# Kernel tuning notes

Measured on AMD Instinct MI355X. Metric: run time of the kernel, lower is better.

Reference implementation:

```python
import jax, jax.numpy as jnp
import numpy as np

EMBED = 2048
HEADS = 16
HEAD_DIM = EMBED // HEADS


def setup_inputs() -> dict:
    key = jax.random.key(0)
    ks = jax.random.split(key, 9)
    s = 1.0 / np.sqrt(EMBED)
    inp = {"x": jax.random.normal(ks[0], (2, 2048, EMBED), dtype=jnp.float32)}
    for i, name in enumerate(["q", "k", "v", "o"]):
        inp[f"W{name}"] = jax.random.uniform(ks[1 + 2 * i], (EMBED, EMBED), dtype=jnp.float32, minval=-s, maxval=s)
        inp[f"b{name}"] = jax.random.uniform(ks[2 + 2 * i], (EMBED,), dtype=jnp.float32, minval=-s, maxval=s)
    return inp


def reference(x, Wq, bq, Wk, bk, Wv, bv, Wo, bo):
    B, S, E = x.shape
    def split_heads(t):
        return t.reshape(B, S, HEADS, HEAD_DIM).transpose(0, 2, 1, 3)  # [B,H,S,D]
    q = split_heads(x @ Wq.T + bq)
    k = split_heads(x @ Wk.T + bk)
    v = split_heads(x @ Wv.T + bv)
    scale = 1.0 / np.sqrt(HEAD_DIM)
    scores = jnp.einsum("bhqd,bhkd->bhqk", q, k) * scale  # [B,H,S,S]
    causal = jnp.tril(jnp.ones((S, S), dtype=bool))
    scores = jnp.where(causal[None, None], scores, -jnp.inf)
    attn = jax.nn.softmax(scores, axis=-1)
    out = jnp.einsum("bhqk,bhkd->bhqd", attn, v)  # [B,H,S,D]
    out = out.transpose(0, 2, 1, 3).reshape(B, S, E)
    return out @ Wo.T + bo
```

## Files before the change

### kernel.cpp

```cpp
#include <hip/hip_runtime.h>

typedef unsigned short u16;
typedef unsigned int u32;
typedef __attribute__((ext_vector_type(8))) short bf16x8;
typedef __attribute__((ext_vector_type(4))) float f32x4;

#define MFMA(a, b, c) __builtin_amdgcn_mfma_f32_16x16x32_bf16((a), (b), (c), 0, 0, 0)

__device__ inline u16 f2bf(float f) {
  u32 u = __float_as_uint(f);
  u = (u + 0x7fffu + ((u >> 16) & 1u)) >> 16;
  return (u16)u;
}

__device__ inline void gld16(u16* lds, const u16* g) {
  __builtin_amdgcn_global_load_lds((const __attribute__((address_space(1))) void*)g,
                                   (__attribute__((address_space(3))) void*)lds,
                                   16, 0, 0);
}

__global__ __launch_bounds__(256) void cvt_all(const float* __restrict__ x,
                                               const float* __restrict__ wa,
                                               const float* __restrict__ wb,
                                               const float* __restrict__ wc,
                                               const float* __restrict__ wd,
                                               uint2* __restrict__ dst) {
  int i = blockIdx.x * 256 + threadIdx.x;
  const float* s;
  int off;
  if (i < 2097152) {
    s = x; off = i;
  } else {
    int j = i - 2097152;
    int which = j >> 20;
    off = j & 1048575;
    s = (which == 0) ? wa : (which == 1) ? wb : (which == 2) ? wc : wd;
  }
  float4 f = ((const float4*)s)[off];
  u32 lo = (u32)f2bf(f.x) | ((u32)f2bf(f.y) << 16);
  u32 hi = (u32)f2bf(f.z) | ((u32)f2bf(f.w) << 16);
  dst[i] = make_uint2(lo, hi);
}

__device__ inline void gemm_core(const u16* __restrict__ A, const u16* __restrict__ W,
                                 u16* As, u16* Bs, int m0, int n0, f32x4 acc[4][4]) {
  const int K = 2048;
  const int NT = 64;
  int t = threadIdx.x, w = t >> 6, l = t & 63;
  int wr = (w >> 1) * 64, wc = (w & 1) * 64;
  int fr = l & 15, fg = l >> 4;
  int r0 = t >> 2;
  int r1 = 64 + r0;
  int c00 = (t & 3) ^ ((r0 >> 1) & 3);
  int c01 = (t & 3) ^ ((r1 >> 1) & 3);
  const u16* gA = A + (size_t)m0 * K;
  const u16* gB = W + (size_t)n0 * K;
  size_t a0 = (size_t)r0 * K + c00 * 8;
  size_t a1 = (size_t)r1 * K + c01 * 8;
#pragma unroll
  for (int p = 0; p < 2; ++p) {
    u16* sa = As + p * 4096;
    u16* sb = Bs + p * 4096;
    int kk = p * 32;
    gld16(sa + w * 512, gA + a0 + kk);
    gld16(sa + 2048 + w * 512, gA + a1 + kk);
    gld16(sb + w * 512, gB + a0 + kk);
    gld16(sb + 2048 + w * 512, gB + a1 + kk);
  }
  for (int kt = 0; kt < NT; ++kt) {
    int kt2 = (kt + 2 < NT) ? (kt + 2) : (NT - 1);
    u16* sa = As + ((kt + 2) & 3) * 4096;
    u16* sb = Bs + ((kt + 2) & 3) * 4096;
    int kk = kt2 * 32;
    gld16(sa + w * 512, gA + a0 + kk);
    gld16(sa + 2048 + w * 512, gA + a1 + kk);
    gld16(sb + w * 512, gB + a0 + kk);
    gld16(sb + 2048 + w * 512, gB + a1 + kk);
    asm volatile("s_waitcnt vmcnt(8)\n\ts_barrier" ::: "memory");
    const u16* ca = As + (kt & 3) * 4096;
    const u16* cb = Bs + (kt & 3) * 4096;
    bf16x8 af[4], bfv[4];
#pragma unroll
    for (int i = 0; i < 4; ++i) {
      int ar = wr + i * 16 + fr;
      af[i] = *(const bf16x8*)&ca[ar * 32 + ((fg ^ ((ar >> 1) & 3)) << 3)];
    }
#pragma unroll
    for (int i = 0; i < 4; ++i) {
      int br = wc + i * 16 + fr;
      bfv[i] = *(const bf16x8*)&cb[br * 32 + ((fg ^ ((br >> 1) & 3)) << 3)];
    }
    __builtin_amdgcn_s_setprio(1);
#pragma unroll
    for (int mi = 0; mi < 4; ++mi)
#pragma unroll
      for (int ni = 0; ni < 4; ++ni)
        acc[mi][ni] = MFMA(af[mi], bfv[ni], acc[mi][ni]);
    __builtin_amdgcn_s_setprio(0);
  }
}

__global__ __launch_bounds__(512, 2) void qkv_gemm(
    const u16* __restrict__ X, const u16* __restrict__ Wq, const u16* __restrict__ Wk,
    const u16* __restrict__ Wv, const float* __restrict__ bq, const float* __restrict__ bk,
    const float* __restrict__ bv, u16* __restrict__ Qo, u16* __restrict__ Ko,
    u16* __restrict__ Vo) {
  __shared__ __attribute__((aligned(16))) u16 As[32768];
  __shared__ __attribute__((aligned(16))) u16 Bs[32768];
  const int K = 2048, NT = 64;
  int which = blockIdx.x >> 3;
  int n0 = (blockIdx.x & 7) * 256;
  int m0 = blockIdx.y * 256;
  const u16* W = (which == 0) ? Wq : (which == 1) ? Wk : Wv;
  const float* bias = (which == 0) ? bq : (which == 1) ? bk : bv;
  u16* out = (which == 0) ? Qo : (which == 1) ? Ko : Vo;
  float scale = (which == 0) ? 0.08838834764831845f : 1.0f;
  int t = threadIdx.x, w = t >> 6, l = t & 63;
  int wm = w >> 2, wn = w & 3;
  int fr = l & 15, fg = l >> 4;
  int r0 = t >> 2;
  int c0 = (t & 3) ^ ((r0 >> 1) & 3);
  const u16* gA = X + (size_t)m0 * K;
  const u16* gB = W + (size_t)n0 * K;
  size_t a0 = (size_t)r0 * K + c0 * 8;
  size_t a1 = a0 + (size_t)128 * K;
  f32x4 zero4 = {0.f, 0.f, 0.f, 0.f};
  f32x4 acc[8][4];
#pragma unroll
  for (int i = 0; i < 8; ++i)
#pragma unroll
    for (int j = 0; j < 4; ++j) acc[i][j] = zero4;
#pragma unroll
  for (int p = 0; p < 2; ++p) {
    u16* sa = As + p * 8192;
    u16* sb = Bs + p * 8192;
    int kk = p * 32;
    gld16(sa + w * 512, gA + a0 + kk);
    gld16(sa + 4096 + w * 512, gA + a1 + kk);
    gld16(sb + w * 512, gB + a0 + kk);
    gld16(sb + 4096 + w * 512, gB + a1 + kk);
  }
  asm volatile("s_waitcnt vmcnt(4)" ::: "memory");
  __builtin_amdgcn_s_barrier();
  for (int kt = 0; kt < NT; ++kt) {
    int kt2 = (kt + 2 < NT) ? (kt + 2) : (NT - 1);
    u16* sa = As + ((kt + 2) & 3) * 8192;
    u16* sb = Bs + ((kt + 2) & 3) * 8192;
    int kk = kt2 * 32;
    const u16* ca = As + (kt & 3) * 8192;
    const u16* cb = Bs + (kt & 3) * 8192;
    bf16x8 af[8], bfv[4];
#pragma unroll
    for (int i = 0; i < 4; ++i) {
      int ar = wm * 128 + i * 16 + fr;
      af[i] = *(const bf16x8*)&ca[ar * 32 + ((fg ^ ((ar >> 1) & 3)) << 3)];
    }
#pragma unroll
    for (int i = 0; i < 4; ++i) {
      int br = wn * 64 + i * 16 + fr;
      bfv[i] = *(const bf16x8*)&cb[br * 32 + ((fg ^ ((br >> 1) & 3)) << 3)];
    }
    gld16(sa + w * 512, gA + a0 + kk);
    gld16(sa + 4096 + w * 512, gA + a1 + kk);
    __builtin_amdgcn_s_barrier();
    __builtin_amdgcn_sched_barrier(0);
    __builtin_amdgcn_s_setprio(1);
#pragma unroll
    for (int mi = 0; mi < 4; ++mi)
#pragma unroll
      for (int ni = 0; ni < 4; ++ni)
        acc[mi][ni] = MFMA(af[mi], bfv[ni], acc[mi][ni]);
    __builtin_amdgcn_s_setprio(0);
    __builtin_amdgcn_sched_barrier(0);
    __builtin_amdgcn_s_barrier();
#pragma unroll
    for (int i = 4; i < 8; ++i) {
      int ar = wm * 128 + i * 16 + fr;
      af[i] = *(const bf16x8*)&ca[ar * 32 + ((fg ^ ((ar >> 1) & 3)) << 3)];
    }
    gld16(sb + w * 512, gB + a0 + kk);
    gld16(sb + 4096 + w * 512, gB + a1 + kk);
    __builtin_amdgcn_s_barrier();
    __builtin_amdgcn_sched_barrier(0);
    __builtin_amdgcn_s_setprio(1);
#pragma unroll
    for (int mi = 4; mi < 8; ++mi)
#pragma unroll
      for (int ni = 0; ni < 4; ++ni)
        acc[mi][ni] = MFMA(af[mi], bfv[ni], acc[mi][ni]);
    __builtin_amdgcn_s_setprio(0);
    __builtin_amdgcn_sched_barrier(0);
    asm volatile("s_waitcnt vmcnt(4)" ::: "memory");
    __builtin_amdgcn_s_barrier();
  }
  if (which == 2) {
#pragma unroll
    for (int mi = 0; mi < 8; ++mi) {
#pragma unroll
      for (int ni = 0; ni < 4; ++ni) {
        int row = m0 + wm * 128 + mi * 16 + (l >> 4) * 4;
        int col = n0 + wn * 64 + ni * 16 + (l & 15);
        float bb = bias[col];
        int h = col >> 7, d = col & 127;
        int b = row >> 11, s = row & 2047;
        u32 p0 = (u32)f2bf(acc[mi][ni][0] + bb) | ((u32)f2bf(acc[mi][ni][1] + bb) << 16);
        u32 p1 = (u32)f2bf(acc[mi][ni][2] + bb) | ((u32)f2bf(acc[mi][ni][3] + bb) << 16);
        *(uint2*)&out[((size_t)(b * 16 + h) * 128 + d) * 2048 + s] = make_uint2(p0, p1);
      }
    }
  } else {
#pragma unroll
    for (int mi = 0; mi < 8; ++mi) {
#pragma unroll
      for (int ni = 0; ni < 4; ++ni) {
        int row = m0 + wm * 128 + mi * 16 + (l >> 4) * 4;
        int col = n0 + wn * 64 + ni * 16 + (l & 15);
        float bb = bias[col];
        int h = col >> 7, d = col & 127;
#pragma unroll
        for (int i = 0; i < 4; ++i) {
          int m = row + i;
          int b = m >> 11, s = m & 2047;
          float v = (acc[mi][ni][i] + bb) * scale;
          out[(((size_t)b * 16 + h) * 2048 + s) * 128 + d] = f2bf(v);
        }
      }
    }
  }
}

__global__ __launch_bounds__(256, 2) void oproj_gemm(const u16* __restrict__ A,
                                                     const u16* __restrict__ W,
                                                     const float* __restrict__ bias,
                                                     float* __restrict__ out) {
  __shared__ __attribute__((aligned(16))) u16 As[16384];
  __shared__ __attribute__((aligned(16))) u16 Bs[16384];
  int n0 = blockIdx.x * 128, m0 = blockIdx.y * 128;
  f32x4 zero4 = {0.f, 0.f, 0.f, 0.f};
  f32x4 acc[4][4];
#pragma unroll
  for (int i = 0; i < 4; ++i)
#pragma unroll
    for (int j = 0; j < 4; ++j) acc[i][j] = zero4;
  gemm_core(A, W, As, Bs, m0, n0, acc);
  int t = threadIdx.x, w = t >> 6, l = t & 63;
  int wr = (w >> 1) * 64, wc = (w & 1) * 64;
#pragma unroll
  for (int mi = 0; mi < 4; ++mi) {
#pragma unroll
    for (int ni = 0; ni < 4; ++ni) {
      int row = m0 + wr + mi * 16 + (l >> 4) * 4;
      int col = n0 + wc + ni * 16 + (l & 15);
      float bb = bias[col];
#pragma unroll
      for (int i = 0; i < 4; ++i) out[(size_t)(row + i) * 2048 + col] = acc[mi][ni][i] + bb;
    }
  }
}

__global__ __launch_bounds__(256, 2) void attn_fwd(const u16* __restrict__ Q,
                                                   const u16* __restrict__ K,
                                                   const u16* __restrict__ Vt,
                                                   u16* __restrict__ AO) {
  __shared__ __attribute__((aligned(16))) u16 Ks[8192];
  __shared__ __attribute__((aligned(16))) u16 Vts[8192];
  __shared__ __attribute__((aligned(16))) u16 Pl[8192];
  const int D = 128;
  int b3 = blockIdx.x;
  int bh = b3 & 31;
  int xq = b3 >> 5;
  int qt = (xq < 8) ? (15 - xq) : (xq - 8);
  int t = threadIdx.x, w = t >> 6, l = t & 63, g = l >> 4, c = l & 15;
  size_t base = (size_t)bh * 2048 * 128;
  const u16* Vbh = Vt + base;
  int q0 = qt * 128;
  int qrw = q0 + w * 32;
  bf16x8 qf[2][4];
#pragma unroll
  for (int mi = 0; mi < 2; ++mi) {
    const u16* qp = Q + base + (size_t)(qrw + mi * 16 + c) * D + g * 8;
#pragma unroll
    for (int ks = 0; ks < 4; ++ks) qf[mi][ks] = *(const bf16x8*)(qp + ks * 32);
  }
  f32x4 zero4 = {0.f, 0.f, 0.f, 0.f};
  f32x4 oacc[2][8];
#pragma unroll
  for (int mi = 0; mi < 2; ++mi)
#pragma unroll
    for (int i = 0; i < 8; ++i) oacc[mi][i] = zero4;
  float mrow[2][4], lrow[2][4];
#pragma unroll
  for (int mi = 0; mi < 2; ++mi)
#pragma unroll
    for (int i = 0; i < 4; ++i) { mrow[mi][i] = -1e30f; lrow[mi][i] = 0.f; }
  char* pw = (char*)(Pl + w * 2048);
  int ktmax = 2 * qt + 1;
  for (int kt = 0; kt <= ktmax; ++kt) {
    int kv0 = kt * 64;
    __syncthreads();
#pragma unroll
    for (int ci = 0; ci < 4; ++ci) {
      int row = w * 16 + ci * 4 + g;
      int cc = c ^ (row & 7);
      gld16(Ks + w * 2048 + ci * 512, K + base + (size_t)(kv0 + row) * D + cc * 8);
    }
#pragma unroll
    for (int ci = 0; ci < 4; ++ci) {
      int vr = ci * 32 + w * 8 + (l >> 3);
      int vslot = (l & 7) ^ ((l >> 3) & 7);
      gld16(Vts + ci * 2048 + w * 512, Vbh + (size_t)vr * 2048 + kv0 + vslot * 8);
    }
    __syncthreads();
    if (kv0 <= qrw + 31) {
      f32x4 sacc[2][4];
#pragma unroll
      for (int mi = 0; mi < 2; ++mi)
#pragma unroll
        for (int n = 0; n < 4; ++n) sacc[mi][n] = zero4;
#pragma unroll
      for (int ks = 0; ks < 4; ++ks) {
#pragma unroll
        for (int n = 0; n < 4; ++n) {
          int row = n * 16 + c;
          bf16x8 kf = *(const bf16x8*)&Ks[row * 128 + (((ks * 4 + g) ^ (c & 7)) << 3)];
          sacc[0][n] = MFMA(qf[0][ks], kf, sacc[0][n]);
          sacc[1][n] = MFMA(qf[1][ks], kf, sacc[1][n]);
        }
      }
      float sc[2][4][4];
#pragma unroll
      for (int mi = 0; mi < 2; ++mi)
#pragma unroll
        for (int n = 0; n < 4; ++n)
#pragma unroll
          for (int i = 0; i < 4; ++i) sc[mi][n][i] = sacc[mi][n][i];
      if (kv0 + 63 > qrw) {
#pragma unroll
        for (int mi = 0; mi < 2; ++mi)
#pragma unroll
          for (int n = 0; n < 4; ++n) {
            int kv = kv0 + n * 16 + c;
#pragma unroll
            for (int i = 0; i < 4; ++i)
              if (kv > qrw + mi * 16 + g * 4 + i) sc[mi][n][i] = -1e30f;
          }
      }
      float tmax[2][4];
#pragma unroll
      for (int mi = 0; mi < 2; ++mi)
#pragma unroll
        for (int i = 0; i < 4; ++i)
          tmax[mi][i] = fmaxf(fmaxf(sc[mi][0][i], sc[mi][1][i]), fmaxf(sc[mi][2][i], sc[mi][3][i]));
#pragma unroll
      for (int x = 1; x < 16; x <<= 1)
#pragma unroll
        for (int mi = 0; mi < 2; ++mi)
#pragma unroll
          for (int i = 0; i < 4; ++i) tmax[mi][i] = fmaxf(tmax[mi][i], __shfl_xor(tmax[mi][i], x));
      float corr[2][4], rs[2][4];
#pragma unroll
      for (int mi = 0; mi < 2; ++mi)
#pragma unroll
        for (int i = 0; i < 4; ++i) {
          float mn = fmaxf(mrow[mi][i], tmax[mi][i]);
          corr[mi][i] = __expf(mrow[mi][i] - mn);
          mrow[mi][i] = mn;
          rs[mi][i] = 0.f;
        }
      float ps[2][4][4];
#pragma unroll
      for (int mi = 0; mi < 2; ++mi)
#pragma unroll
        for (int n = 0; n < 4; ++n)
#pragma unroll
          for (int i = 0; i < 4; ++i) {
            ps[mi][n][i] = __expf(sc[mi][n][i] - mrow[mi][i]);
            rs[mi][i] += ps[mi][n][i];
          }
#pragma unroll
      for (int x = 1; x < 16; x <<= 1)
#pragma unroll
        for (int mi = 0; mi < 2; ++mi)
#pragma unroll
          for (int i = 0; i < 4; ++i) rs[mi][i] += __shfl_xor(rs[mi][i], x);
#pragma unroll
      for (int mi = 0; mi < 2; ++mi)
#pragma unroll
        for (int i = 0; i < 4; ++i) lrow[mi][i] = lrow[mi][i] * corr[mi][i] + rs[mi][i];
#pragma unroll
      for (int mi = 0; mi < 2; ++mi)
#pragma unroll
        for (int nf = 0; nf < 8; ++nf)
#pragma unroll
          for (int i = 0; i < 4; ++i) oacc[mi][nf][i] *= corr[mi][i];
#pragma unroll
      for (int mi = 0; mi < 2; ++mi)
#pragma unroll
        for (int n = 0; n < 4; ++n)
#pragma unroll
          for (int i = 0; i < 4; ++i) {
            int row = mi * 16 + g * 4 + i;
            *(u16*)(pw + row * 128 + ((n * 32 + c * 2) ^ ((row & 7) << 4))) = f2bf(ps[mi][n][i]);
          }
#pragma unroll
      for (int ks = 0; ks < 2; ++ks) {
        bf16x8 pf0 = *(const bf16x8*)(pw + (c)*128 + ((ks * 64 + g * 16) ^ ((c & 7) << 4)));
        bf16x8 pf1 = *(const bf16x8*)(pw + (16 + c) * 128 + ((ks * 64 + g * 16) ^ ((c & 7) << 4)));
#pragma unroll
        for (int nf = 0; nf < 8; ++nf) {
          bf16x8 vf = *(const bf16x8*)&Vts[(nf * 16 + c) * 64 + (((ks * 4 + g) ^ (c & 7)) << 3)];
          oacc[0][nf] = MFMA(pf0, vf, oacc[0][nf]);
          oacc[1][nf] = MFMA(pf1, vf, oacc[1][nf]);
        }
      }
    }
  }
  int b = bh >> 4, h = bh & 15;
#pragma unroll
  for (int mi = 0; mi < 2; ++mi)
#pragma unroll
    for (int nf = 0; nf < 8; ++nf) {
      int d = h * 128 + nf * 16 + c;
#pragma unroll
      for (int i = 0; i < 4; ++i) {
        int q = qrw + mi * 16 + g * 4 + i;
        AO[((size_t)b * 2048 + q) * 2048 + d] = f2bf(oacc[mi][nf][i] / lrow[mi][i]);
      }
    }
}

extern "C" void kernel_launch(void* const* d_in, const int* in_sizes, int n_in,
                              void* d_out, int out_size, void* d_ws, size_t ws_size,
                              hipStream_t stream) {
  const float* x = (const float*)d_in[0];
  const float* Wq = (const float*)d_in[1];
  const float* bq = (const float*)d_in[2];
  const float* Wk = (const float*)d_in[3];
  const float* bk = (const float*)d_in[4];
  const float* Wv = (const float*)d_in[5];
  const float* bv = (const float*)d_in[6];
  const float* Wo = (const float*)d_in[7];
  const float* bo = (const float*)d_in[8];
  float* out = (float*)d_out;

  u16* xb = (u16*)d_ws;
  u16* Wqb = xb + 8388608;
  u16* Wkb = Wqb + 4194304;
  u16* Wvb = Wkb + 4194304;
  u16* Wob = Wvb + 4194304;
  u16* Qb = Wob + 4194304;
  u16* Kb = Qb + 8388608;
  u16* Vb = Kb + 8388608;
  u16* AOb = xb;

  cvt_all<<<24576, 256, 0, stream>>>(x, Wq, Wk, Wv, Wo, (uint2*)d_ws);
  qkv_gemm<<<dim3(24, 16), 512, 0, stream>>>(xb, Wqb, Wkb, Wvb, bq, bk, bv, Qb, Kb, Vb);
  attn_fwd<<<512, 256, 0, stream>>>(Qb, Kb, Vb, AOb);
  oproj_gemm<<<dim3(16, 32), 256, 0, stream>>>(AOb, Wob, bo, out);
}
```

Before: 288.2 us.

## Restructure QKV GEMM main loop into double-buffered 64-wide K steps

The QKV projection GEMM main loop now covers 64 K-elements per iteration as two 32-wide sub-steps, and uses two LDS halves in ping-pong order instead of a four-slot ring with prefetch distance two. The A-fragment register array shrinks from 8 to 4 entries and is reloaded for the upper rows, which lowers register pressure. Explicit lgkmcnt waits are placed before each MFMA block, and the vmcnt wait moves to sit after each B prefetch. The goal is fewer loop iterations and less bookkeeping. In exchange the prefetch distance is shorter and there are more barriers per iteration.

```diff
diff --git a/kernel.cpp b/kernel.cpp
--- a/kernel.cpp
+++ b/kernel.cpp
@@ -107,7 +107,7 @@
     u16* __restrict__ Vo) {
   __shared__ __attribute__((aligned(16))) u16 As[32768];
   __shared__ __attribute__((aligned(16))) u16 Bs[32768];
-  const int K = 2048, NT = 64;
+  const int K = 2048, NT = 32;
   int which = blockIdx.x >> 3;
   int n0 = (blockIdx.x & 7) * 256;
   int m0 = blockIdx.y * 256;
@@ -118,8 +118,8 @@
   int t = threadIdx.x, w = t >> 6, l = t & 63;
   int wm = w >> 2, wn = w & 3;
   int fr = l & 15, fg = l >> 4;
-  int r0 = t >> 2;
-  int c0 = (t & 3) ^ ((r0 >> 1) & 3);
+  int r0 = t >> 2, sl = t & 3;
+  int c0 = sl ^ ((r0 >> 1) & 3);
   const u16* gA = X + (size_t)m0 * K;
   const u16* gB = W + (size_t)n0 * K;
   size_t a0 = (size_t)r0 * K + c0 * 8;
@@ -130,26 +130,23 @@
   for (int i = 0; i < 8; ++i)
 #pragma unroll
     for (int j = 0; j < 4; ++j) acc[i][j] = zero4;
-#pragma unroll
-  for (int p = 0; p < 2; ++p) {
-    u16* sa = As + p * 8192;
-    u16* sb = Bs + p * 8192;
-    int kk = p * 32;
-    gld16(sa + w * 512, gA + a0 + kk);
-    gld16(sa + 4096 + w * 512, gA + a1 + kk);
-    gld16(sb + w * 512, gB + a0 + kk);
-    gld16(sb + 4096 + w * 512, gB + a1 + kk);
-  }
+  gld16(As + w * 512, gA + a0);
+  gld16(As + 4096 + w * 512, gA + a1);
+  gld16(Bs + w * 512, gB + a0);
+  gld16(Bs + 4096 + w * 512, gB + a1);
+  gld16(As + 8192 + w * 512, gA + a0 + 32);
+  gld16(As + 8192 + 4096 + w * 512, gA + a1 + 32);
+  gld16(Bs + 8192 + w * 512, gB + a0 + 32);
+  gld16(Bs + 8192 + 4096 + w * 512, gB + a1 + 32);
   asm volatile("s_waitcnt vmcnt(4)" ::: "memory");
   __builtin_amdgcn_s_barrier();
-  for (int kt = 0; kt < NT; ++kt) {
-    int kt2 = (kt + 2 < NT) ? (kt + 2) : (NT - 1);
-    u16* sa = As + ((kt + 2) & 3) * 8192;
-    u16* sb = Bs + ((kt + 2) & 3) * 8192;
-    int kk = kt2 * 32;
-    const u16* ca = As + (kt & 3) * 8192;
-    const u16* cb = Bs + (kt & 3) * 8192;
-    bf16x8 af[8], bfv[4];
+  for (int T = 0; T < NT; ++T) {
+    const u16* ca = As + (T & 1) * 16384;
+    const u16* cb = Bs + (T & 1) * 16384;
+    int Ts = (T + 1 < NT) ? (T + 1) : T;
+    int so = ((T + 1) & 1) * 16384;
+    size_t gk = (size_t)Ts * 64;
+    bf16x8 af[4], bfv[4];
 #pragma unroll
     for (int i = 0; i < 4; ++i) {
       int ar = wm * 128 + i * 16 + fr;
@@ -160,9 +157,10 @@
       int br = wn * 64 + i * 16 + fr;
       bfv[i] = *(const bf16x8*)&cb[br * 32 + ((fg ^ ((br >> 1) & 3)) << 3)];
     }
-    gld16(sa + w * 512, gA + a0 + kk);
-    gld16(sa + 4096 + w * 512, gA + a1 + kk);
-    __builtin_amdgcn_s_barrier();
+    gld16(As + so + w * 512, gA + a0 + gk);
+    gld16(As + so + 4096 + w * 512, gA + a1 + gk);
+    __builtin_amdgcn_s_barrier();
+    asm volatile("s_waitcnt lgkmcnt(0)" ::: "memory");
     __builtin_amdgcn_sched_barrier(0);
     __builtin_amdgcn_s_setprio(1);
 #pragma unroll
@@ -174,23 +172,68 @@
     __builtin_amdgcn_sched_barrier(0);
     __builtin_amdgcn_s_barrier();
 #pragma unroll
-    for (int i = 4; i < 8; ++i) {
+    for (int i = 0; i < 4; ++i) {
+      int ar = wm * 128 + (i + 4) * 16 + fr;
+      af[i] = *(const bf16x8*)&ca[ar * 32 + ((fg ^ ((ar >> 1) & 3)) << 3)];
+    }
+    gld16(Bs + so + w * 512, gB + a0 + gk);
+    gld16(Bs + so + 4096 + w * 512, gB + a1 + gk);
+    asm volatile("s_waitcnt vmcnt(4)" ::: "memory");
+    __builtin_amdgcn_s_barrier();
+    asm volatile("s_waitcnt lgkmcnt(0)" ::: "memory");
+    __builtin_amdgcn_sched_barrier(0);
+    __builtin_amdgcn_s_setprio(1);
+#pragma unroll
+    for (int mi = 0; mi < 4; ++mi)
+#pragma unroll
+      for (int ni = 0; ni < 4; ++ni)
+        acc[mi + 4][ni] = MFMA(af[mi], bfv[ni], acc[mi + 4][ni]);
+    __builtin_amdgcn_s_setprio(0);
+    __builtin_amdgcn_sched_barrier(0);
+    __builtin_amdgcn_s_barrier();
+#pragma unroll
+    for (int i = 0; i < 4; ++i) {
       int ar = wm * 128 + i * 16 + fr;
-      af[i] = *(const bf16x8*)&ca[ar * 32 + ((fg ^ ((ar >> 1) & 3)) << 3)];
-    }
-    gld16(sb + w * 512, gB + a0 + kk);
-    gld16(sb + 4096 + w * 512, gB + a1 + kk);
-    __builtin_amdgcn_s_barrier();
+      af[i] = *(const bf16x8*)&ca[8192 + ar * 32 + ((fg ^ ((ar >> 1) & 3)) << 3)];
+    }
+#pragma unroll
+    for (int i = 0; i < 4; ++i) {
+      int br = wn * 64 + i * 16 + fr;
+      bfv[i] = *(const bf16x8*)&cb[8192 + br * 32 + ((fg ^ ((br >> 1) & 3)) << 3)];
+    }
+    gld16(As + so + 8192 + w * 512, gA + a0 + gk + 32);
+    gld16(As + so + 8192 + 4096 + w * 512, gA + a1 + gk + 32);
+    __builtin_amdgcn_s_barrier();
+    asm volatile("s_waitcnt lgkmcnt(0)" ::: "memory");
     __builtin_amdgcn_sched_barrier(0);
     __builtin_amdgcn_s_setprio(1);
 #pragma unroll
-    for (int mi = 4; mi < 8; ++mi)
+    for (int mi = 0; mi < 4; ++mi)
 #pragma unroll
       for (int ni = 0; ni < 4; ++ni)
         acc[mi][ni] = MFMA(af[mi], bfv[ni], acc[mi][ni]);
     __builtin_amdgcn_s_setprio(0);
     __builtin_amdgcn_sched_barrier(0);
+    __builtin_amdgcn_s_barrier();
+#pragma unroll
+    for (int i = 0; i < 4; ++i) {
+      int ar = wm * 128 + (i + 4) * 16 + fr;
+      af[i] = *(const bf16x8*)&ca[8192 + ar * 32 + ((fg ^ ((ar >> 1) & 3)) << 3)];
+    }
+    gld16(Bs + so + 8192 + w * 512, gB + a0 + gk + 32);
+    gld16(Bs + so + 8192 + 4096 + w * 512, gB + a1 + gk + 32);
     asm volatile("s_waitcnt vmcnt(4)" ::: "memory");
+    __builtin_amdgcn_s_barrier();
+    asm volatile("s_waitcnt lgkmcnt(0)" ::: "memory");
+    __builtin_amdgcn_sched_barrier(0);
+    __builtin_amdgcn_s_setprio(1);
+#pragma unroll
+    for (int mi = 0; mi < 4; ++mi)
+#pragma unroll
+      for (int ni = 0; ni < 4; ++ni)
+        acc[mi + 4][ni] = MFMA(af[mi], bfv[ni], acc[mi + 4][ni]);
+    __builtin_amdgcn_s_setprio(0);
+    __builtin_amdgcn_sched_barrier(0);
     __builtin_amdgcn_s_barrier();
   }
   if (which == 2) {
```

New measurement: 316.6 us. 9.9% more time.
